# Optimization experiments

Measured on AMD Instinct MI355X. Metric: run time of the kernel, lower is better.

## Reference

```python
import jax, jax.numpy as jnp
import numpy as np

COMMITMENT_COST = 0.25


def setup_inputs() -> dict:
    key = jax.random.key(0)
    k1, k2 = jax.random.split(key)
    inputs = jax.random.normal(k1, (16, 256, 32, 32), dtype=jnp.float32)
    embedding = jax.random.normal(k2, (8192, 256), dtype=jnp.float32)
    return {"inputs": inputs, "embedding": embedding}


def reference(inputs, embedding):
    # inputs: [B, C, H, W] with C == embedding_dim; embedding: [K, C]
    B, C, H, W = inputs.shape
    x = jnp.transpose(inputs, (0, 2, 3, 1))          # [B, H, W, C]
    flat = x.reshape(-1, C)                           # [N, C]
    # squared L2 distances: ||f||^2 + ||e||^2 - 2 f.e
    dist = (jnp.sum(flat * flat, axis=1, keepdims=True)
            + jnp.sum(embedding * embedding, axis=1)
            - 2.0 * flat @ embedding.T)               # [N, K]
    idx = jnp.argmin(dist, axis=1)                    # [N]
    quantized = embedding[idx].reshape(x.shape)       # [B, H, W, C]
    # commitment loss (eval mode: no EMA buffer updates)
    e_latent_loss = jnp.mean((jax.lax.stop_gradient(quantized) - x) ** 2)
    loss = COMMITMENT_COST * e_latent_loss
    # straight-through estimator
    q_st = x + jax.lax.stop_gradient(quantized - x)
    out = jnp.transpose(q_st, (0, 3, 1, 2))           # [B, C, H, W]
    return out, loss, idx.reshape(B, -1)
```

## Files before the change

### kernel.cpp

```cpp
#include <hip/hip_runtime.h>

#define C_   256
#define HW_  1024
#define N_   16384
#define K_   8192
#define OUT_SZ   4194304
#define LOSS_OFF 4194304
#define IDX_OFF  4194305
#define MARGIN   0.3f

typedef __attribute__((ext_vector_type(8)))  short short8;
typedef __attribute__((ext_vector_type(4)))  float f32x4;

#define BH_OFF     0u
#define CNORM_OFF  4194304u
#define NCNORM_OFF 4227072u
#define LIST_OFF   4259840u
#define CNT_OFF    4325376u
#define FIDX_OFF   4325440u
#define WS_NEED    4390976u

#define FB_CNORM   0u
#define FB_BESTS   32768u
#define FB_BESTK   557056u
#define FB_FIDX    1081344u

__device__ __forceinline__ unsigned short f2bf_rne(float x) {
  unsigned u = __float_as_uint(x);
  unsigned r = (u + 0x7fffu + ((u >> 16) & 1u)) >> 16;
  return (unsigned short)r;
}
__device__ __forceinline__ float bf2f(unsigned short h) {
  return __uint_as_float(((unsigned)h) << 16);
}
__device__ __forceinline__ void gld16(const void* g, void* l) {
  __builtin_amdgcn_global_load_lds((const __attribute__((address_space(1))) unsigned*)g,
                                   (__attribute__((address_space(3))) unsigned*)l, 16, 0, 0);
}
__device__ __forceinline__ float med3(float a, float b, float c) {
#if __has_builtin(__builtin_amdgcn_fmed3f)
  return __builtin_amdgcn_fmed3f(a, b, c);
#else
  return fmaxf(fminf(fmaxf(a, b), c), fminf(a, b));
#endif
}

__global__ __launch_bounds__(256) void conv_fused(const float* __restrict__ inp,
                                                  const float* __restrict__ emb,
                                                  unsigned short* __restrict__ Ah,
                                                  unsigned short* __restrict__ Bh,
                                                  float* __restrict__ cnorm,
                                                  float* __restrict__ ncnorm,
                                                  float* __restrict__ loss_slot,
                                                  int* __restrict__ counter) {
  __shared__ float T[64][65];
  int tid = threadIdx.x;
  if (blockIdx.x < 2048) {
    int wave = tid >> 6, lane = tid & 63;
    int k = blockIdx.x * 4 + wave;
    float4 v = *(const float4*)(emb + (size_t)k * C_ + lane * 4);
    float ss = v.x*v.x + v.y*v.y + v.z*v.z + v.w*v.w;
    #pragma unroll
    for (int m = 32; m > 0; m >>= 1) ss += __shfl_xor(ss, m);
    if (lane == 0) { cnorm[k] = 0.5f * ss; ncnorm[k] = -0.5f * ss; }
    uint2 p;
    p.x = (unsigned)f2bf_rne(v.x) | ((unsigned)f2bf_rne(v.y) << 16);
    p.y = (unsigned)f2bf_rne(v.z) | ((unsigned)f2bf_rne(v.w) << 16);
    *(uint2*)&Bh[(size_t)k * C_ + lane * 4] = p;
    if (blockIdx.x == 0 && tid == 0) { *loss_slot = 0.0f; *counter = 0; }
  } else {
    int bb = blockIdx.x - 2048;
    int nt = bb >> 2, ct = bb & 3;
    int n0 = nt * 64, c0 = ct * 64;
    int b = n0 >> 10, hw0 = n0 & 1023;
    const float* base = inp + (size_t)b * (C_ * HW_) + hw0;
    #pragma unroll
    for (int i = 0; i < 16; ++i) {
      int cl = i * 4 + (tid >> 6), nl = tid & 63;
      T[nl][cl] = base[(size_t)(c0 + cl) * HW_ + nl];
    }
    __syncthreads();
    #pragma unroll
    for (int i = 0; i < 16; ++i) {
      int nl = i * 4 + (tid >> 6), cl = tid & 63;
      Ah[(size_t)(n0 + nl) * C_ + c0 + cl] = f2bf_rne(T[nl][cl]);
    }
  }
}

__global__ __launch_bounds__(256, 2) void k_gemm1p(const unsigned short* __restrict__ Ah,
                                                   const unsigned short* __restrict__ Bh,
                                                   const float* __restrict__ ncnorm,
                                                   uint4* __restrict__ Rec) {
  __shared__ __align__(16) unsigned short LDS[3][12288];
  __shared__ __align__(16) float ncnL[1024];
  __shared__ float mS[2][128][3];

  const int tid = threadIdx.x, lane = tid & 63, wave = tid >> 6;
  const int wr = wave >> 1, wc = wave & 1;
  const int bid = (int)blockIdx.x;
  const int wg = (bid & 7) * 128 + (bid >> 3);
  const int rb = wg >> 3, kb = wg & 7;
  const int row0 = rb * 128;
  const int qm = lane & 15, quad = lane >> 4;
  const int sw = (quad ^ ((qm >> 1) & 3)) * 8;

  const char* srcA[2]; int dstA[2];
  #pragma unroll
  for (int t = 0; t < 2; ++t) {
    int g = t * 256 + tid;
    int row = g >> 2, chs = g & 3, ch = chs ^ ((row >> 1) & 3);
    srcA[t] = (const char*)Ah + (size_t)(row0 + row) * 512 + ch * 16;
    dstA[t] = g * 16;
  }
  const char* srcB[4]; int dstB[4];
  #pragma unroll
  for (int t = 0; t < 4; ++t) {
    int g = t * 256 + tid;
    int r = g >> 2, chs = g & 3, ch = chs ^ ((r >> 1) & 3);
    srcB[t] = (const char*)Bh + (size_t)(kb * 1024 + r) * 512 + ch * 16;
    dstB[t] = 8192 + g * 16;
  }

  gld16((const char*)ncnorm + (size_t)kb * 4096 + tid * 16, (char*)ncnL + tid * 16);
  #pragma unroll
  for (int t = 0; t < 2; ++t) gld16(srcA[t], (char*)LDS[0] + dstA[t]);
  #pragma unroll
  for (int t = 0; t < 4; ++t) gld16(srcB[t], (char*)LDS[0] + dstB[t]);
  #pragma unroll
  for (int t = 0; t < 2; ++t) gld16(srcA[t] + 64, (char*)LDS[1] + dstA[t]);
  #pragma unroll
  for (int t = 0; t < 4; ++t) gld16(srcB[t] + 64, (char*)LDS[1] + dstB[t]);
  asm volatile("s_waitcnt vmcnt(12)" ::: "memory");
  __builtin_amdgcn_s_barrier();

  const unsigned wq  = (unsigned)(wc * 128 + quad * 4);
  const unsigned kmk = 0xFFFFFF00u;

  int cur = 0, nst = 2;

  for (int sub = 0; sub < 4; ++sub) {
    const int nbe = kb * 4 + sub;
    const int nb4 = sub * 256 + wc * 128 + quad * 4;
    f32x4 acc[4][8];
    {
      float4 ncn[8];
      #pragma unroll
      for (int ct = 0; ct < 8; ++ct) ncn[ct] = *(const float4*)&ncnL[nb4 + ct * 16];
      #pragma unroll
      for (int r = 0; r < 4; ++r)
        #pragma unroll
        for (int c = 0; c < 8; ++c) {
          acc[r][c][0] = ncn[c].x; acc[r][c][1] = ncn[c].y;
          acc[r][c][2] = ncn[c].z; acc[r][c][3] = ncn[c].w;
        }
    }

    #pragma unroll 2
    for (int ci = 0; ci < 8; ++ci) {
      const int it = (sub << 3) | ci;
      if (it < 31) asm volatile("s_waitcnt vmcnt(6)" ::: "memory");
      else         asm volatile("s_waitcnt vmcnt(0)" ::: "memory");
      __builtin_amdgcn_s_barrier();
      __builtin_amdgcn_sched_barrier(0);

      if (it + 2 < 32) {
        const int nt2 = it + 2, nsub = nt2 >> 3, nci = nt2 & 7;
        #pragma unroll
        for (int t = 0; t < 2; ++t)
          gld16(srcA[t] + nci * 64, (char*)LDS[nst] + dstA[t]);
        #pragma unroll
        for (int t = 0; t < 4; ++t)
          gld16(srcB[t] + (size_t)nsub * 131072 + nci * 64, (char*)LDS[nst] + dstB[t]);
      }

      const unsigned short* Lb = &LDS[cur][0];
      short8 ah[4];
      #pragma unroll
      for (int rt = 0; rt < 4; ++rt) {
        int row = (wr * 4 + rt) * 16 + qm;
        ah[rt] = *(const short8*)&Lb[row * 32 + sw];
      }
      __builtin_amdgcn_s_setprio(1);
      #pragma unroll
      for (int ch2 = 0; ch2 < 2; ++ch2) {
        short8 bh[4];
        #pragma unroll
        for (int q = 0; q < 4; ++q) {
          int ct = ch2 * 4 + q;
          int r = (wc * 8 + ct) * 16 + qm;
          bh[q] = *(const short8*)&Lb[4096 + r * 32 + sw];
        }
        #pragma unroll
        for (int rt = 0; rt < 4; ++rt)
          #pragma unroll
          for (int q = 0; q < 4; ++q)
            acc[rt][ch2 * 4 + q] =
              __builtin_amdgcn_mfma_f32_16x16x32_bf16(bh[q], ah[rt], acc[rt][ch2 * 4 + q], 0, 0, 0);
      }
      __builtin_amdgcn_s_setprio(0);
      cur = (cur == 2) ? 0 : cur + 1;
      nst = (nst == 2) ? 0 : nst + 1;
    }

    #pragma unroll
    for (int rt = 0; rt < 4; ++rt) {
      float t1 = -3.4e38f, t2 = t1, t3 = t1;
      #pragma unroll
      for (int ct = 0; ct < 8; ++ct)
        #pragma unroll
        for (int rg = 0; rg < 4; ++rg) {
          unsigned idxv = wq | (unsigned)(ct * 16 + rg);
          float kf = __uint_as_float((__float_as_uint(acc[rt][ct][rg]) & kmk) | idxv);
          float n3 = med3(t2, kf, t3);
          float n2 = med3(t1, kf, t2);
          t1 = fmaxf(t1, kf);
          t2 = n2; t3 = n3;
        }
      #pragma unroll
      for (int m = 16; m < 64; m <<= 1) {
        float b1 = __shfl_xor(t1, m), b2 = __shfl_xor(t2, m), b3 = __shfl_xor(t3, m);
        float n3 = med3(t2, b1, t3);
        float n2 = med3(t1, b1, t2);
        t1 = fmaxf(t1, b1); t2 = n2; t3 = n3;
        n3 = med3(t2, b2, t3); t2 = fmaxf(t2, b2); t3 = n3;
        t3 = fmaxf(t3, b3);
      }
      if (quad == 0) {
        int rowl = wr * 64 + rt * 16 + qm;
        mS[wc][rowl][0] = t1; mS[wc][rowl][1] = t2; mS[wc][rowl][2] = t3;
      }
    }
    asm volatile("s_waitcnt lgkmcnt(0)" ::: "memory");
    __builtin_amdgcn_s_barrier();
    __builtin_amdgcn_sched_barrier(0);
    if (tid < 128) {
      float s1 = mS[0][tid][0], s2 = mS[0][tid][1], s3 = mS[0][tid][2];
      float b1 = mS[1][tid][0], b2 = mS[1][tid][1], b3 = mS[1][tid][2];
      float n3 = med3(s2, b1, s3);
      float n2 = med3(s1, b1, s2);
      s1 = fmaxf(s1, b1); s2 = n2; s3 = n3;
      n3 = med3(s2, b2, s3); s2 = fmaxf(s2, b2); s3 = n3;
      s3 = fmaxf(s3, b3);
      unsigned u1 = __float_as_uint(s1), u2 = __float_as_uint(s2), u3 = __float_as_uint(s3);
      uint4 rec;
      rec.x = u1 & kmk;
      rec.y = ((unsigned)f2bf_rne(__uint_as_float(u2 & kmk)) << 16)
            |  (unsigned)f2bf_rne(__uint_as_float(u3 & kmk));
      rec.z = (u1 & 255u) | ((u2 & 255u) << 8) | ((u3 & 255u) << 16);
      rec.w = 0u;
      Rec[(size_t)nbe * N_ + row0 + tid] = rec;
    }
  }
}

__global__ __launch_bounds__(64) void k_merge3(const uint4* __restrict__ Rec,
                                               int* __restrict__ fidx,
                                               float* __restrict__ outIdx,
                                               int* __restrict__ list,
                                               int* __restrict__ counter) {
  int row = blockIdx.x * 64 + threadIdx.x;
  float g1 = -3.4e38f; int gk = 0;
  #pragma unroll
  for (int s = 0; s < 32; ++s) {
    uint4 v = Rec[(size_t)s * N_ + row];
    float s1 = __uint_as_float(v.x);
    if (s1 > g1) { g1 = s1; gk = s * 256 + (int)(v.z & 255u); }
  }
  float thr = g1 - MARGIN;
  int cnt = 0;
  #pragma unroll
  for (int s = 0; s < 32; ++s) {
    uint4 v = Rec[(size_t)s * N_ + row];
    cnt += (__uint_as_float(v.x) >= thr);
    cnt += (bf2f((unsigned short)(v.y >> 16)) >= thr);
    cnt += (bf2f((unsigned short)(v.y & 0xffffu)) >= thr);
  }
  if (cnt == 1) { fidx[row] = gk; outIdx[row] = (float)gk; }
  else { int p = atomicAdd(counter, 1); list[p] = row; }
}

__global__ __launch_bounds__(256) void k_refine(const float* __restrict__ inp,
                                                const float* __restrict__ emb,
                                                const float* __restrict__ cnorm,
                                                const uint4* __restrict__ Rec,
                                                const int* __restrict__ list,
                                                const int* __restrict__ counter,
                                                int* __restrict__ fidx,
                                                float* __restrict__ outIdx) {
  __shared__ float f[256];
  __shared__ float ls1[32];
  __shared__ int   ck[96];
  __shared__ float csc[96];
  __shared__ int   ncand;
  int tid = threadIdx.x, lane = tid & 63, wv = tid >> 6;
  int count = *counter;
  for (int i = blockIdx.x; i < count; i += 1024) {
    int row = list[i];
    __syncthreads();
    f[tid] = inp[(size_t)(row >> 10) * (C_ * HW_) + (size_t)tid * HW_ + (row & 1023)];
    if (tid == 0) ncand = 0;
    if (tid < 32) ls1[tid] = __uint_as_float(Rec[(size_t)tid * N_ + row].x);
    __syncthreads();
    float g1 = ls1[0];
    #pragma unroll
    for (int s = 1; s < 32; ++s) g1 = fmaxf(g1, ls1[s]);
    float thr = g1 - MARGIN;
    if (tid < 32) {
      uint4 v = Rec[(size_t)tid * N_ + row];
      float s1 = __uint_as_float(v.x);
      float s2 = bf2f((unsigned short)(v.y >> 16));
      float s3 = bf2f((unsigned short)(v.y & 0xffffu));
      int b = tid * 256;
      if (s1 >= thr) { int p = atomicAdd(&ncand, 1); ck[p] = b + (int)(v.z & 255u); }
      if (s2 >= thr) { int p = atomicAdd(&ncand, 1); ck[p] = b + (int)((v.z >> 8) & 255u); }
      if (s3 >= thr) { int p = atomicAdd(&ncand, 1); ck[p] = b + (int)((v.z >> 16) & 255u); }
    }
    __syncthreads();
    int nc = ncand;
    for (int c = wv; c < nc; c += 4) {
      int k = ck[c];
      float4 e = ((const float4*)(emb + (size_t)k * C_))[lane];
      float d = f[lane*4]*e.x + f[lane*4+1]*e.y + f[lane*4+2]*e.z + f[lane*4+3]*e.w;
      #pragma unroll
      for (int m = 32; m > 0; m >>= 1) d += __shfl_xor(d, m);
      if (lane == 0) csc[c] = d - cnorm[k];
    }
    __syncthreads();
    if (tid == 0) {
      float bs = csc[0]; int bk = ck[0];
      for (int c = 1; c < nc; ++c)
        if (csc[c] > bs || (csc[c] == bs && ck[c] < bk)) { bs = csc[c]; bk = ck[c]; }
      fidx[row] = bk; outIdx[row] = (float)bk;
    }
    __syncthreads();
  }
}

__global__ __launch_bounds__(256) void k_out(const float* __restrict__ inp,
                                             const float* __restrict__ emb,
                                             const int* __restrict__ fidx,
                                             float* __restrict__ out,
                                             float* __restrict__ loss) {
  __shared__ float Q[32][260];
  int tid = threadIdx.x;
  int n0 = blockIdx.x * 32, b = n0 >> 10, hw0 = n0 & 1023;
  #pragma unroll
  for (int p = 0; p < 8; ++p) {
    int r = p * 4 + (tid >> 6);
    int kq = fidx[n0 + r];
    float4 v = *(const float4*)(emb + (size_t)kq * C_ + (tid & 63) * 4);
    *(float4*)&Q[r][(tid & 63) * 4] = v;
  }
  __syncthreads();
  int hwl = tid & 31, cl = tid >> 5;
  float lsum = 0.0f;
  #pragma unroll
  for (int p = 0; p < 32; ++p) {
    int c = p * 8 + cl;
    size_t a = (size_t)b * (C_ * HW_) + (size_t)c * HW_ + hw0 + hwl;
    float q = Q[hwl][c];
    float x = inp[a];
    out[a] = q;
    float dd = q - x; lsum += dd * dd;
  }
  #pragma unroll
  for (int m = 32; m > 0; m >>= 1) lsum += __shfl_xor(lsum, m);
  __shared__ float red[4];
  if ((tid & 63) == 0) red[tid >> 6] = lsum;
  __syncthreads();
  if (tid == 0)
    atomicAdd(loss, (red[0] + red[1] + red[2] + red[3]) * (0.25f / (float)OUT_SZ));
}

__global__ __launch_bounds__(256) void k_norms_fb(const float* __restrict__ emb,
                                                  float* __restrict__ cnorm,
                                                  float* __restrict__ loss_slot) {
  int tid = threadIdx.x, wave = tid >> 6, lane = tid & 63;
  int k = blockIdx.x * 4 + wave;
  float4 v = *(const float4*)(emb + k * C_ + lane * 4);
  float s = v.x*v.x + v.y*v.y + v.z*v.z + v.w*v.w;
  #pragma unroll
  for (int m = 32; m > 0; m >>= 1) s += __shfl_xor(s, m);
  if (lane == 0) cnorm[k] = 0.5f * s;
  if (blockIdx.x == 0 && tid == 0) *loss_slot = 0.0f;
}

__global__ __launch_bounds__(256) void k_score_fb(const float* __restrict__ inp,
                                                  const float* __restrict__ emb,
                                                  const float* __restrict__ cnorm,
                                                  float* __restrict__ bestS,
                                                  int*   __restrict__ bestK) {
  __shared__ float As[16][132];
  __shared__ float Bs[16][132];
  const int tid = threadIdx.x;
  const int tx = tid & 15, ty = tid >> 4;
  const int rt = blockIdx.x >> 3, ks = blockIdx.x & 7;
  const int row0 = rt * 128;
  const float* Abase = inp + (row0 >> 10) * (C_ * HW_) + (row0 & 1023);
  const int kbase = ks * 1024;
  const int m4  = (tid & 31) << 2;
  const int ccA = tid >> 5;
  const int cc4 = (tid & 3) << 2;
  const int kkB = tid >> 2;

  float rS[8]; int rK[8];
  #pragma unroll
  for (int r = 0; r < 8; ++r) { rS[r] = -3.4e38f; rK[r] = 0; }

  for (int kt = 0; kt < 8; ++kt) {
    const int k0 = kbase + kt * 128;
    float acc[8][8];
    #pragma unroll
    for (int r = 0; r < 8; ++r)
      #pragma unroll
      for (int c = 0; c < 8; ++c) acc[r][c] = 0.f;

    for (int ci = 0; ci < 16; ++ci) {
      const int c0 = ci * 16;
      __syncthreads();
      #pragma unroll
      for (int p = 0; p < 2; ++p) {
        int cc = ccA + p * 8;
        float4 v = *(const float4*)(Abase + (c0 + cc) * HW_ + m4);
        *(float4*)(&As[cc][m4]) = v;
      }
      #pragma unroll
      for (int p = 0; p < 2; ++p) {
        int k = kkB + p * 64;
        float4 v = *(const float4*)(emb + (size_t)(k0 + k) * C_ + c0 + cc4);
        Bs[cc4 + 0][k] = v.x; Bs[cc4 + 1][k] = v.y;
        Bs[cc4 + 2][k] = v.z; Bs[cc4 + 3][k] = v.w;
      }
      __syncthreads();
      #pragma unroll
      for (int cc = 0; cc < 16; ++cc) {
        float4 a0 = *(const float4*)(&As[cc][ty * 8]);
        float4 a1 = *(const float4*)(&As[cc][ty * 8 + 4]);
        float4 b0 = *(const float4*)(&Bs[cc][tx * 8]);
        float4 b1 = *(const float4*)(&Bs[cc][tx * 8 + 4]);
        float a[8] = {a0.x, a0.y, a0.z, a0.w, a1.x, a1.y, a1.z, a1.w};
        float b[8] = {b0.x, b0.y, b0.z, b0.w, b1.x, b1.y, b1.z, b1.w};
        #pragma unroll
        for (int r = 0; r < 8; ++r)
          #pragma unroll
          for (int c = 0; c < 8; ++c) acc[r][c] += a[r] * b[c];
      }
    }
    float cn[8];
    {
      float4 c0v = *(const float4*)(cnorm + k0 + tx * 8);
      float4 c1v = *(const float4*)(cnorm + k0 + tx * 8 + 4);
      cn[0] = c0v.x; cn[1] = c0v.y; cn[2] = c0v.z; cn[3] = c0v.w;
      cn[4] = c1v.x; cn[5] = c1v.y; cn[6] = c1v.z; cn[7] = c1v.w;
    }
    #pragma unroll
    for (int r = 0; r < 8; ++r)
      #pragma unroll
      for (int c = 0; c < 8; ++c) {
        float s = acc[r][c] - cn[c];
        if (s > rS[r]) { rS[r] = s; rK[r] = k0 + tx * 8 + c; }
      }
  }
  #pragma unroll
  for (int r = 0; r < 8; ++r) {
    float s = rS[r]; int kk = rK[r];
    #pragma unroll
    for (int m = 1; m < 16; m <<= 1) {
      float so = __shfl_xor(s, m);
      int   ko = __shfl_xor(kk, m);
      if (so > s || (so == s && ko < kk)) { s = so; kk = ko; }
    }
    if (tx == 0) {
      int row = row0 + ty * 8 + r;
      bestS[ks * N_ + row] = s;
      bestK[ks * N_ + row] = kk;
    }
  }
}

__global__ __launch_bounds__(256) void k_merge_fb(const float* __restrict__ bestS,
                                                  const int*   __restrict__ bestK,
                                                  float* __restrict__ out_idx,
                                                  int*   __restrict__ fidx) {
  int n = blockIdx.x * 256 + threadIdx.x;
  float bs = -3.4e38f; int bk = 0x7fffffff;
  #pragma unroll
  for (int s = 0; s < 8; ++s) {
    float v = bestS[s * N_ + n];
    int  kk = bestK[s * N_ + n];
    if (v > bs || (v == bs && kk < bk)) { bs = v; bk = kk; }
  }
  out_idx[n] = (float)bk;
  fidx[n] = bk;
}

extern "C" void kernel_launch(void* const* d_in, const int* in_sizes, int n_in,
                              void* d_out, int out_size, void* d_ws, size_t ws_size,
                              hipStream_t stream) {
  const float* inp = (const float*)d_in[0];
  const float* emb = (const float*)d_in[1];
  float* out = (float*)d_out;
  char* ws = (char*)d_ws;

  if (ws_size >= (size_t)WS_NEED) {
    unsigned short* Ah = (unsigned short*)d_out;
    uint4* Rec = (uint4*)((char*)d_out + 8388608u);
    unsigned short* Bh = (unsigned short*)(ws + BH_OFF);
    float* cnorm   = (float*)(ws + CNORM_OFF);
    float* ncnorm  = (float*)(ws + NCNORM_OFF);
    int*   list    = (int*)(ws + LIST_OFF);
    int*   counter = (int*)(ws + CNT_OFF);
    int*   fidx    = (int*)(ws + FIDX_OFF);

    conv_fused <<<3072,   256, 0, stream>>>(inp, emb, Ah, Bh, cnorm, ncnorm,
                                            out + LOSS_OFF, counter);
    k_gemm1p   <<<1024,   256, 0, stream>>>(Ah, Bh, ncnorm, Rec);
    k_merge3   <<<N_/64,  64,  0, stream>>>(Rec, fidx, out + IDX_OFF, list, counter);
    k_refine   <<<1024,   256, 0, stream>>>(inp, emb, cnorm, Rec, list, counter,
                                            fidx, out + IDX_OFF);
    k_out      <<<N_/32,  256, 0, stream>>>(inp, emb, fidx, out, out + LOSS_OFF);
  } else {
    float* cnorm = (float*)(ws + FB_CNORM);
    float* bestS = (float*)(ws + FB_BESTS);
    int*   bestK = (int*)(ws + FB_BESTK);
    int*   fidx  = (int*)(ws + FB_FIDX);

    k_norms_fb <<<K_ / 4, 256, 0, stream>>>(emb, cnorm, out + LOSS_OFF);
    k_score_fb <<<1024,   256, 0, stream>>>(inp, emb, cnorm, bestS, bestK);
    k_merge_fb <<<N_/256, 256, 0, stream>>>(bestS, bestK, out + IDX_OFF, fidx);
    k_out      <<<OUT_SZ/8192, 256, 0, stream>>>(inp, emb, fidx, out, out + LOSS_OFF);
  }
}
```

Measured before the change: 187.3 us.

## Fuse merge, refine and output kernels into one per-tile post kernel

Replaces the three post-GEMM kernels (merge3, refine with global atomic list, out) with a single k_post kernel per 64-row tile. The candidate merge uses 4 threads per row with shuffle reduction. Ambiguous rows are refined inside the block, and the gather/transpose/loss writes use float4 stores. This removes two launches, the global counter/list/fidx traffic and the grid-wide refine loop. The cost is serialised per-block refinement of ambiguous rows and a larger LDS tile that may lower occupancy. Rec moves to the workspace and Bh to the output buffer.

After: 183.3 us. 1.02x faster.

```diff
diff --git a/kernel.cpp b/kernel.cpp
--- a/kernel.cpp
+++ b/kernel.cpp
@@ -12,13 +12,10 @@
 typedef __attribute__((ext_vector_type(8)))  short short8;
 typedef __attribute__((ext_vector_type(4)))  float f32x4;
 
-#define BH_OFF     0u
-#define CNORM_OFF  4194304u
-#define NCNORM_OFF 4227072u
-#define LIST_OFF   4259840u
-#define CNT_OFF    4325376u
-#define FIDX_OFF   4325440u
-#define WS_NEED    4390976u
+#define REC_OFF    0u
+#define CNORM_OFF  8388608u
+#define NCNORM_OFF 8421376u
+#define WS_NEED    8454144u
 
 #define FB_CNORM   0u
 #define FB_BESTS   32768u
@@ -51,8 +48,7 @@
                                                   unsigned short* __restrict__ Bh,
                                                   float* __restrict__ cnorm,
                                                   float* __restrict__ ncnorm,
-                                                  float* __restrict__ loss_slot,
-                                                  int* __restrict__ counter) {
+                                                  float* __restrict__ loss_slot) {
   __shared__ float T[64][65];
   int tid = threadIdx.x;
   if (blockIdx.x < 2048) {
@@ -67,7 +63,7 @@
     p.x = (unsigned)f2bf_rne(v.x) | ((unsigned)f2bf_rne(v.y) << 16);
     p.y = (unsigned)f2bf_rne(v.z) | ((unsigned)f2bf_rne(v.w) << 16);
     *(uint2*)&Bh[(size_t)k * C_ + lane * 4] = p;
-    if (blockIdx.x == 0 && tid == 0) { *loss_slot = 0.0f; *counter = 0; }
+    if (blockIdx.x == 0 && tid == 0) { *loss_slot = 0.0f; }
   } else {
     int bb = blockIdx.x - 2048;
     int nt = bb >> 2, ct = bb & 3;
@@ -254,70 +250,83 @@
   }
 }
 
-__global__ __launch_bounds__(64) void k_merge3(const uint4* __restrict__ Rec,
-                                               int* __restrict__ fidx,
-                                               float* __restrict__ outIdx,
-                                               int* __restrict__ list,
-                                               int* __restrict__ counter) {
-  int row = blockIdx.x * 64 + threadIdx.x;
-  float g1 = -3.4e38f; int gk = 0;
-  #pragma unroll
-  for (int s = 0; s < 32; ++s) {
-    uint4 v = Rec[(size_t)s * N_ + row];
-    float s1 = __uint_as_float(v.x);
-    if (s1 > g1) { g1 = s1; gk = s * 256 + (int)(v.z & 255u); }
-  }
-  float thr = g1 - MARGIN;
+__global__ __launch_bounds__(256) void k_post(const float* __restrict__ inp,
+                                              const float* __restrict__ emb,
+                                              const float* __restrict__ cnorm,
+                                              const uint4* __restrict__ Rec,
+                                              float* __restrict__ out,
+                                              float* __restrict__ outIdx,
+                                              float* __restrict__ loss) {
+  __shared__ float Q[64][259];
+  __shared__ float gS[64];
+  __shared__ int   ridx[64];
+  __shared__ int   flist[64];
+  __shared__ float f[256];
+  __shared__ int   ck[96];
+  __shared__ float csc[96];
+  __shared__ int   nflag, ncand;
+  __shared__ float red[4];
+
+  const int tid = threadIdx.x;
+  const int n0 = blockIdx.x * 64, b = n0 >> 10, hw0 = n0 & 1023;
+
+  const int r = tid >> 2, j = tid & 3;
+  const int row = n0 + r;
+  uint4 rv[8];
+  #pragma unroll
+  for (int q = 0; q < 8; ++q) rv[q] = Rec[(size_t)(j * 8 + q) * N_ + row];
+  float m1 = -3.4e38f; int gk = 0x7fffffff;
+  #pragma unroll
+  for (int q = 0; q < 8; ++q) {
+    float s1 = __uint_as_float(rv[q].x);
+    int  kk = (j * 8 + q) * 256 + (int)(rv[q].z & 255u);
+    if (s1 > m1) { m1 = s1; gk = kk; }
+  }
+  #pragma unroll
+  for (int m = 1; m < 4; m <<= 1) {
+    float so = __shfl_xor(m1, m); int ko = __shfl_xor(gk, m);
+    if (so > m1 || (so == m1 && ko < gk)) { m1 = so; gk = ko; }
+  }
+  float thr = m1 - MARGIN;
   int cnt = 0;
   #pragma unroll
-  for (int s = 0; s < 32; ++s) {
-    uint4 v = Rec[(size_t)s * N_ + row];
+  for (int q = 0; q < 8; ++q) {
+    uint4 v = rv[q];
     cnt += (__uint_as_float(v.x) >= thr);
     cnt += (bf2f((unsigned short)(v.y >> 16)) >= thr);
     cnt += (bf2f((unsigned short)(v.y & 0xffffu)) >= thr);
   }
-  if (cnt == 1) { fidx[row] = gk; outIdx[row] = (float)gk; }
-  else { int p = atomicAdd(counter, 1); list[p] = row; }
-}
-
-__global__ __launch_bounds__(256) void k_refine(const float* __restrict__ inp,
-                                                const float* __restrict__ emb,
-                                                const float* __restrict__ cnorm,
-                                                const uint4* __restrict__ Rec,
-                                                const int* __restrict__ list,
-                                                const int* __restrict__ counter,
-                                                int* __restrict__ fidx,
-                                                float* __restrict__ outIdx) {
-  __shared__ float f[256];
-  __shared__ float ls1[32];
-  __shared__ int   ck[96];
-  __shared__ float csc[96];
-  __shared__ int   ncand;
-  int tid = threadIdx.x, lane = tid & 63, wv = tid >> 6;
-  int count = *counter;
-  for (int i = blockIdx.x; i < count; i += 1024) {
-    int row = list[i];
+  cnt += __shfl_xor(cnt, 1); cnt += __shfl_xor(cnt, 2);
+  if (tid == 0) nflag = 0;
+  __syncthreads();
+  if (j == 0) {
+    gS[r] = m1;
+    if (cnt == 1) { ridx[r] = gk; }
+    else { ridx[r] = -1; int p = atomicAdd(&nflag, 1); flist[p] = r; }
+  }
+  __syncthreads();
+
+  int nf = nflag;
+  for (int i = 0; i < nf; ++i) {
+    int lr = flist[i];
+    int rw = n0 + lr;
+    f[tid] = inp[(size_t)(rw >> 10) * (C_ * HW_) + (size_t)tid * HW_ + (rw & 1023)];
+    if (tid == 0) ncand = 0;
     __syncthreads();
-    f[tid] = inp[(size_t)(row >> 10) * (C_ * HW_) + (size_t)tid * HW_ + (row & 1023)];
-    if (tid == 0) ncand = 0;
-    if (tid < 32) ls1[tid] = __uint_as_float(Rec[(size_t)tid * N_ + row].x);
-    __syncthreads();
-    float g1 = ls1[0];
-    #pragma unroll
-    for (int s = 1; s < 32; ++s) g1 = fmaxf(g1, ls1[s]);
-    float thr = g1 - MARGIN;
+    float th2 = gS[lr] - MARGIN;
     if (tid < 32) {
-      uint4 v = Rec[(size_t)tid * N_ + row];
+      uint4 v = Rec[(size_t)tid * N_ + rw];
       float s1 = __uint_as_float(v.x);
       float s2 = bf2f((unsigned short)(v.y >> 16));
       float s3 = bf2f((unsigned short)(v.y & 0xffffu));
-      int b = tid * 256;
-      if (s1 >= thr) { int p = atomicAdd(&ncand, 1); ck[p] = b + (int)(v.z & 255u); }
-      if (s2 >= thr) { int p = atomicAdd(&ncand, 1); ck[p] = b + (int)((v.z >> 8) & 255u); }
-      if (s3 >= thr) { int p = atomicAdd(&ncand, 1); ck[p] = b + (int)((v.z >> 16) & 255u); }
+      int bb = tid * 256;
+      if (s1 >= th2) { int p = atomicAdd(&ncand, 1); ck[p] = bb + (int)(v.z & 255u); }
+      if (s2 >= th2) { int p = atomicAdd(&ncand, 1); ck[p] = bb + (int)((v.z >> 8) & 255u); }
+      if (s3 >= th2) { int p = atomicAdd(&ncand, 1); ck[p] = bb + (int)((v.z >> 16) & 255u); }
     }
     __syncthreads();
     int nc = ncand;
+    int lane = tid & 63, wv = tid >> 6;
     for (int c = wv; c < nc; c += 4) {
       int k = ck[c];
       float4 e = ((const float4*)(emb + (size_t)k * C_))[lane];
@@ -331,42 +340,38 @@
       float bs = csc[0]; int bk = ck[0];
       for (int c = 1; c < nc; ++c)
         if (csc[c] > bs || (csc[c] == bs && ck[c] < bk)) { bs = csc[c]; bk = ck[c]; }
-      fidx[row] = bk; outIdx[row] = (float)bk;
+      ridx[lr] = bk;
     }
     __syncthreads();
   }
-}
-
-__global__ __launch_bounds__(256) void k_out(const float* __restrict__ inp,
-                                             const float* __restrict__ emb,
-                                             const int* __restrict__ fidx,
-                                             float* __restrict__ out,
-                                             float* __restrict__ loss) {
-  __shared__ float Q[32][260];
-  int tid = threadIdx.x;
-  int n0 = blockIdx.x * 32, b = n0 >> 10, hw0 = n0 & 1023;
+
+  if (tid < 64) outIdx[n0 + tid] = (float)ridx[tid];
   #pragma unroll
   for (int p = 0; p < 8; ++p) {
-    int r = p * 4 + (tid >> 6);
-    int kq = fidx[n0 + r];
-    float4 v = *(const float4*)(emb + (size_t)kq * C_ + (tid & 63) * 4);
-    *(float4*)&Q[r][(tid & 63) * 4] = v;
+    int rr = p * 8 + (tid >> 5);
+    int kq = ridx[rr];
+    int l8 = (tid & 31) * 8;
+    *(float4*)&Q[rr][l8]     = *(const float4*)(emb + (size_t)kq * C_ + l8);
+    *(float4*)&Q[rr][l8 + 4] = *(const float4*)(emb + (size_t)kq * C_ + l8 + 4);
   }
   __syncthreads();
-  int hwl = tid & 31, cl = tid >> 5;
+
   float lsum = 0.0f;
-  #pragma unroll
-  for (int p = 0; p < 32; ++p) {
-    int c = p * 8 + cl;
-    size_t a = (size_t)b * (C_ * HW_) + (size_t)c * HW_ + hw0 + hwl;
-    float q = Q[hwl][c];
-    float x = inp[a];
-    out[a] = q;
-    float dd = q - x; lsum += dd * dd;
+  const int hw4 = (tid & 15) * 4, cl = tid >> 4;
+  #pragma unroll
+  for (int p = 0; p < 16; ++p) {
+    int c = p * 16 + cl;
+    size_t a = (size_t)b * (C_ * HW_) + (size_t)c * HW_ + hw0 + hw4;
+    float4 x = *(const float4*)(inp + a);
+    float4 q;
+    q.x = Q[hw4 + 0][c]; q.y = Q[hw4 + 1][c];
+    q.z = Q[hw4 + 2][c]; q.w = Q[hw4 + 3][c];
+    *(float4*)(out + a) = q;
+    float d0 = q.x - x.x, d1 = q.y - x.y, d2 = q.z - x.z, d3 = q.w - x.w;
+    lsum += d0*d0 + d1*d1 + d2*d2 + d3*d3;
   }
   #pragma unroll
   for (int m = 32; m > 0; m >>= 1) lsum += __shfl_xor(lsum, m);
-  __shared__ float red[4];
   if ((tid & 63) == 0) red[tid >> 6] = lsum;
   __syncthreads();
   if (tid == 0)
@@ -495,6 +500,42 @@
   fidx[n] = bk;
 }
 
+__global__ __launch_bounds__(256) void k_out_fb(const float* __restrict__ inp,
+                                                const float* __restrict__ emb,
+                                                const int* __restrict__ fidx,
+                                                float* __restrict__ out,
+                                                float* __restrict__ loss) {
+  __shared__ float Q[32][260];
+  int tid = threadIdx.x;
+  int n0 = blockIdx.x * 32, b = n0 >> 10, hw0 = n0 & 1023;
+  #pragma unroll
+  for (int p = 0; p < 8; ++p) {
+    int r = p * 4 + (tid >> 6);
+    int kq = fidx[n0 + r];
+    float4 v = *(const float4*)(emb + (size_t)kq * C_ + (tid & 63) * 4);
+    *(float4*)&Q[r][(tid & 63) * 4] = v;
+  }
+  __syncthreads();
+  int hwl = tid & 31, cl = tid >> 5;
+  float lsum = 0.0f;
+  #pragma unroll
+  for (int p = 0; p < 32; ++p) {
+    int c = p * 8 + cl;
+    size_t a = (size_t)b * (C_ * HW_) + (size_t)c * HW_ + hw0 + hwl;
+    float q = Q[hwl][c];
+    float x = inp[a];
+    out[a] = q;
+    float dd = q - x; lsum += dd * dd;
+  }
+  #pragma unroll
+  for (int m = 32; m > 0; m >>= 1) lsum += __shfl_xor(lsum, m);
+  __shared__ float red[4];
+  if ((tid & 63) == 0) red[tid >> 6] = lsum;
+  __syncthreads();
+  if (tid == 0)
+    atomicAdd(loss, (red[0] + red[1] + red[2] + red[3]) * (0.25f / (float)OUT_SZ));
+}
+
 extern "C" void kernel_launch(void* const* d_in, const int* in_sizes, int n_in,
                               void* d_out, int out_size, void* d_ws, size_t ws_size,
                               hipStream_t stream) {
@@ -505,21 +546,16 @@
 
   if (ws_size >= (size_t)WS_NEED) {
     unsigned short* Ah = (unsigned short*)d_out;
-    uint4* Rec = (uint4*)((char*)d_out + 8388608u);
-    unsigned short* Bh = (unsigned short*)(ws + BH_OFF);
+    unsigned short* Bh = (unsigned short*)((char*)d_out + 8388608u);
+    uint4* Rec     = (uint4*)(ws + REC_OFF);
     float* cnorm   = (float*)(ws + CNORM_OFF);
     float* ncnorm  = (float*)(ws + NCNORM_OFF);
-    int*   list    = (int*)(ws + LIST_OFF);
-    int*   counter = (int*)(ws + CNT_OFF);
-    int*   fidx    = (int*)(ws + FIDX_OFF);
-
-    conv_fused <<<3072,   256, 0, stream>>>(inp, emb, Ah, Bh, cnorm, ncnorm,
-                                            out + LOSS_OFF, counter);
-    k_gemm1p   <<<1024,   256, 0, stream>>>(Ah, Bh, ncnorm, Rec);
-    k_merge3   <<<N_/64,  64,  0, stream>>>(Rec, fidx, out + IDX_OFF, list, counter);
-    k_refine   <<<1024,   256, 0, stream>>>(inp, emb, cnorm, Rec, list, counter,
-                                            fidx, out + IDX_OFF);
-    k_out      <<<N_/32,  256, 0, stream>>>(inp, emb, fidx, out, out + LOSS_OFF);
+
+    conv_fused <<<3072,  256, 0, stream>>>(inp, emb, Ah, Bh, cnorm, ncnorm,
+                                           out + LOSS_OFF);
+    k_gemm1p   <<<1024,  256, 0, stream>>>(Ah, Bh, ncnorm, Rec);
+    k_post     <<<N_/64, 256, 0, stream>>>(inp, emb, cnorm, Rec, out,
+                                           out + IDX_OFF, out + LOSS_OFF);
   } else {
     float* cnorm = (float*)(ws + FB_CNORM);
     float* bestS = (float*)(ws + FB_BESTS);
@@ -529,6 +565,6 @@
     k_norms_fb <<<K_ / 4, 256, 0, stream>>>(emb, cnorm, out + LOSS_OFF);
     k_score_fb <<<1024,   256, 0, stream>>>(inp, emb, cnorm, bestS, bestK);
     k_merge_fb <<<N_/256, 256, 0, stream>>>(bestS, bestK, out + IDX_OFF, fidx);
-    k_out      <<<OUT_SZ/8192, 256, 0, stream>>>(inp, emb, fidx, out, out + LOSS_OFF);
-  }
-}
+    k_out_fb   <<<N_/32,  256, 0, stream>>>(inp, emb, fidx, out, out + LOSS_OFF);
+  }
+}
```
